# Performance work log

Measured on AMD Instinct MI355X. Metric: run time of the kernel, lower is better.

## Reference

```python
import jax, jax.numpy as jnp
import numpy as np
from jax import lax
import math

B, C_IN, C_OUT, D, H, W = 8, 32, 32, 16, 64, 64
K = 3            # kernel_size (cubic)
PAD = 1
E = 8            # num_experts
GROUPS = 1


def setup_inputs() -> dict:
    key = jax.random.key(0)
    k1, k2, k3, k4 = jax.random.split(key, 4)
    x = jax.random.normal(k1, (B, C_IN, D, H, W), dtype=jnp.float32)
    routing_weights = jax.random.uniform(k2, (B, E), dtype=jnp.float32)
    # kaiming_uniform_(a=sqrt(5)) equivalent bounds
    fan_in = (C_IN // GROUPS) * K * K * K
    gain = math.sqrt(2.0 / (1.0 + 5.0))
    w_bound = gain * math.sqrt(3.0 / fan_in)
    weight = jax.random.uniform(k3, (E, C_OUT, C_IN // GROUPS, K, K, K),
                                dtype=jnp.float32, minval=-w_bound, maxval=w_bound)
    b_bound = 1.0 / math.sqrt(fan_in)
    bias = jax.random.uniform(k4, (E, C_OUT), dtype=jnp.float32,
                              minval=-b_bound, maxval=b_bound)
    return {"x": x, "routing_weights": routing_weights, "weight": weight, "bias": bias}


def reference(x, routing_weights, weight, bias):
    # Faithful to the original einsum: 'bi,eocdwh->bocdwh' sums i and e
    # independently (outer-sum semantics), exactly as torch.einsum does.
    eff_kernel = jnp.einsum('bi,eocdwh->bocdwh', routing_weights, weight)  # [B,O,I/g,kd,kh,kw]
    eff_bias = jnp.einsum('bi,eo->bo', routing_weights, bias)              # [B,O]

    def conv_one(xi, ki, bi):
        # xi: [C_in,D,H,W]; ki: [O, I/g, kd,kh,kw]
        y = lax.conv_general_dilated(
            xi[None], ki,
            window_strides=(1, 1, 1),
            padding=[(PAD, PAD)] * 3,
            lhs_dilation=(1, 1, 1),
            rhs_dilation=(1, 1, 1),
            dimension_numbers=('NCDHW', 'OIDHW', 'NCDHW'),
            feature_group_count=GROUPS,
        )[0]
        return y + bi[:, None, None, None]

    return jax.vmap(conv_one)(x, eff_kernel, eff_bias)  # [B, C_OUT, D, H, W]
```

## Files before the change

### kernel.cpp

```cpp
#include <hip/hip_runtime.h>
#include <hip/hip_bf16.h>

typedef short short8 __attribute__((ext_vector_type(8)));
typedef float f32x4 __attribute__((ext_vector_type(4)));

#define WF_OFF  0u
#define RWB_OFF 55296u
#define RWS_OFF 56320u

#define CHS 384
#define RB  1552
#define PLANE_B (10 * RB)
#define RING_B (4 * PLANE_B)

__device__ __forceinline__ unsigned bf16rne(float f) {
    unsigned u = __float_as_uint(f);
    return (u + 0x7FFFu + ((u >> 16) & 1u)) >> 16;
}

__global__ void condconv_prep(const float* __restrict__ rw,
                              const float* __restrict__ weight,
                              const float* __restrict__ bias,
                              char* __restrict__ ws) {
    int i = blockIdx.x * 256 + threadIdx.x;
    if (i < 27648) {
        int t   = i >> 10;
        int rem = i & 1023;
        int ot  = rem >> 9;
        int l   = (rem >> 3) & 63;
        int j   = rem & 7;
        int o   = ot * 16 + (l & 15);
        int c   = 8 * (l >> 4) + j;
        float s = 0.f;
#pragma unroll
        for (int e = 0; e < 8; ++e) s += weight[((e * 32 + o) * 32 + c) * 27 + t];
        ((unsigned short*)(ws + WF_OFF))[i] = (unsigned short)bf16rne(s);
    } else if (i < 27904) {
        int k = i - 27648;
        int b = k >> 5, o = k & 31;
        float rs = 0.f, bs = 0.f;
#pragma unroll
        for (int e = 0; e < 8; ++e) { rs += rw[b * 8 + e]; bs += bias[e * 32 + o]; }
        ((float*)(ws + RWB_OFF))[k] = rs * bs;
        if (o == 0) ((float*)(ws + RWS_OFF))[b] = rs;
    }
}

__global__ __launch_bounds__(256, 2) void condconv_zwalk3(
        const float* __restrict__ x,
        const char* __restrict__ wf,
        const float* __restrict__ rwbias,
        const float* __restrict__ rwsum,
        float* __restrict__ out) {
    __shared__ __align__(16) char smem[RING_B];

    const int tid  = threadIdx.x;
    const int wv   = tid >> 6;
    const int lane = tid & 63;
    const int n    = lane & 15;
    const int quad = lane >> 4;
    const int ot   = wv & 1;
    const int yh   = wv >> 1;

    const int logical = (blockIdx.x & 7) * 64 + (blockIdx.x >> 3);
    const int b   = logical >> 6;
    const int rem = logical & 63;
    const int zb  = rem & 1;
    const int xb  = (rem >> 1) & 3;
    const int yb  = rem >> 3;
    const int y0 = yb * 8, x0 = xb * 16, zr0 = zb * 8;

    const float* xbp = x + (size_t)b * 2097152;

    const bool sact = tid < 240;
    const int  scc  = tid / 60;
    const int  rr   = tid % 60;
    const int  syp  = rr / 6;
    const int  sx4  = rr % 6;
    const int  gxq  = xb * 4 + sx4 - 1;
    const int  gy   = y0 + syp - 1;
    const bool gok  = ((unsigned)gxq < 16u) && ((unsigned)gy < 64u);
    const long soff = (long)scc * 524288 +
                      (long)(gok ? gy : 0) * 64 + (long)(gok ? gxq : 0) * 4;
    const int  woff = syp * RB + scc * CHS + (4 * sx4) * 16;

    short8 wreg[27];
    {
        const char* wb_ = wf + lane * 16 + ot * 1024;
#pragma unroll
        for (int t = 0; t < 27; ++t) wreg[t] = *(const short8*)(wb_ + t * 2048);
    }

    const float rwb = rwsum[b];
    float bb[4];
#pragma unroll
    for (int j = 0; j < 4; ++j) bb[j] = rwbias[b * 32 + ot * 16 + quad * 4 + j];
    float* outb = out + (size_t)(b * 32 + ot * 16 + quad * 4) * 65536 +
                  (size_t)(y0 + yh * 4) * 64 + x0 + n;

    auto STAGE = [&](int p) {
        if (!sact) return;
        char* pl = smem + (p & 3) * PLANE_B;
        float a[8][4];
        if (gok && (unsigned)p < 16u) {
            const float* q0 = xbp + soff + (long)p * 4096;
#pragma unroll
            for (int k = 0; k < 8; ++k) {
                const float4 v = *(const float4*)(q0 + (size_t)k * 65536);
                a[k][0] = v.x; a[k][1] = v.y; a[k][2] = v.z; a[k][3] = v.w;
            }
        } else {
#pragma unroll
            for (int k = 0; k < 8; ++k)
                { a[k][0] = 0.f; a[k][1] = 0.f; a[k][2] = 0.f; a[k][3] = 0.f; }
        }
#pragma unroll
        for (int xi = 0; xi < 4; ++xi) {
            union { __hip_bfloat162 h2[4]; uint4 u; } g;
            g.h2[0] = __float22bfloat162_rn(make_float2(a[0][xi], a[1][xi]));
            g.h2[1] = __float22bfloat162_rn(make_float2(a[2][xi], a[3][xi]));
            g.h2[2] = __float22bfloat162_rn(make_float2(a[4][xi], a[5][xi]));
            g.h2[3] = __float22bfloat162_rn(make_float2(a[6][xi], a[7][xi]));
            *(uint4*)(pl + woff + xi * 16) = g.u;
        }
    };

    STAGE(zr0 - 1);
    STAGE(zr0);

    f32x4 accA[4] = {}, accB[4] = {};

#pragma unroll 1
    for (int k = 0; k < 4; ++k) {
        const int zA = zr0 + 2 * k;

        __syncthreads();
        STAGE(zA + 1);
        STAGE(zA + 2);
        __syncthreads();

#pragma unroll
        for (int pi = 0; pi < 4; ++pi) {
            const char* Pp = smem + ((zA - 1 + pi) & 3) * PLANE_B;
#pragma unroll
            for (int q = 0; q < 6; ++q) {
                const char* rowq = Pp + (yh * 4 + q) * RB + quad * CHS;
#pragma unroll
                for (int dx = 0; dx < 3; ++dx) {
                    const int lx = n + dx + 3;
                    const short8 xf = *(const short8*)(rowq + lx * 16);
#pragma unroll
                    for (int dy = 0; dy < 3; ++dy) {
                        const int r = q - dy;
                        if (r >= 0 && r < 4) {
                            if (pi < 3)
                                accA[r] = __builtin_amdgcn_mfma_f32_16x16x32_bf16(
                                    wreg[pi * 9 + dy * 3 + dx], xf, accA[r], 0, 0, 0);
                            if (pi > 0)
                                accB[r] = __builtin_amdgcn_mfma_f32_16x16x32_bf16(
                                    wreg[(pi - 1) * 9 + dy * 3 + dx], xf, accB[r], 0, 0, 0);
                        }
                    }
                }
            }
        }

#pragma unroll
        for (int r = 0; r < 4; ++r) {
#pragma unroll
            for (int j = 0; j < 4; ++j) {
                float* po = outb + (size_t)j * 65536 + r * 64;
                po[(size_t)zA * 4096]       = rwb * accA[r][j] + bb[j];
                po[(size_t)(zA + 1) * 4096] = rwb * accB[r][j] + bb[j];
            }
            accA[r] = f32x4{0, 0, 0, 0};
            accB[r] = f32x4{0, 0, 0, 0};
        }
    }
}

extern "C" void kernel_launch(void* const* d_in, const int* in_sizes, int n_in,
                              void* d_out, int out_size, void* d_ws, size_t ws_size,
                              hipStream_t stream) {
    const float* x      = (const float*)d_in[0];
    const float* rw     = (const float*)d_in[1];
    const float* weight = (const float*)d_in[2];
    const float* bias   = (const float*)d_in[3];
    float* out = (float*)d_out;
    char*  ws  = (char*)d_ws;

    condconv_prep<<<109, 256, 0, stream>>>(rw, weight, bias, ws);
    condconv_zwalk3<<<512, 256, 0, stream>>>(
        x, ws + WF_OFF,
        (const float*)(ws + RWB_OFF), (const float*)(ws + RWS_OFF), out);
}
```

Measured before the change: 144.3 us.

## Prefetch next z-planes into registers to overlap global loads with MFMA

Splits plane staging into a global load into registers and a later LDS write, so the loads for the next two z-planes are issued before the compute phase and finish while the MFMAs run. It also replaces __syncthreads with raw s_barrier calls fenced by sched_barrier, and adds an explicit lgkmcnt wait so the barriers do not wait on outstanding global loads. The cost is 64 extra VGPRs for the prefetch buffers alongside the 27 weight registers. That pressure could cause spills under launch_bounds(256,2).

```diff
diff --git a/kernel.cpp b/kernel.cpp
--- a/kernel.cpp
+++ b/kernel.cpp
@@ -12,6 +12,11 @@
 #define RB  1552
 #define PLANE_B (10 * RB)
 #define RING_B (4 * PLANE_B)
+
+#define SCHED0() __builtin_amdgcn_sched_barrier(0)
+#define BAR_RAW()  do { SCHED0(); __builtin_amdgcn_s_barrier(); SCHED0(); } while (0)
+#define BAR_LGKM() do { SCHED0(); asm volatile("s_waitcnt lgkmcnt(0)" ::: "memory"); \
+                        __builtin_amdgcn_s_barrier(); SCHED0(); } while (0)
 
 __device__ __forceinline__ unsigned bf16rne(float f) {
     unsigned u = __float_as_uint(f);
@@ -46,7 +51,7 @@
     }
 }
 
-__global__ __launch_bounds__(256, 2) void condconv_zwalk3(
+__global__ __launch_bounds__(256, 2) void condconv_zwalk4(
         const float* __restrict__ x,
         const char* __restrict__ wf,
         const float* __restrict__ rwbias,
@@ -98,21 +103,29 @@
     float* outb = out + (size_t)(b * 32 + ot * 16 + quad * 4) * 65536 +
                   (size_t)(y0 + yh * 4) * 64 + x0 + n;
 
-    auto STAGE = [&](int p) {
+    float4 pX[8], pY[8];
+
+    auto SLOAD = [&](int p, float4 (&dst)[8]) {
+        if (!sact) return;
+        if (gok && (unsigned)p < 16u) {
+            const float* q0 = xbp + soff + (long)p * 4096;
+#pragma unroll
+            for (int kk = 0; kk < 8; ++kk)
+                dst[kk] = *(const float4*)(q0 + (size_t)kk * 65536);
+        } else {
+#pragma unroll
+            for (int kk = 0; kk < 8; ++kk)
+                dst[kk] = make_float4(0.f, 0.f, 0.f, 0.f);
+        }
+    };
+    auto SWRITE = [&](int p, const float4 (&v)[8]) {
         if (!sact) return;
         char* pl = smem + (p & 3) * PLANE_B;
         float a[8][4];
-        if (gok && (unsigned)p < 16u) {
-            const float* q0 = xbp + soff + (long)p * 4096;
-#pragma unroll
-            for (int k = 0; k < 8; ++k) {
-                const float4 v = *(const float4*)(q0 + (size_t)k * 65536);
-                a[k][0] = v.x; a[k][1] = v.y; a[k][2] = v.z; a[k][3] = v.w;
-            }
-        } else {
-#pragma unroll
-            for (int k = 0; k < 8; ++k)
-                { a[k][0] = 0.f; a[k][1] = 0.f; a[k][2] = 0.f; a[k][3] = 0.f; }
+#pragma unroll
+        for (int kk = 0; kk < 8; ++kk) {
+            a[kk][0] = v[kk].x; a[kk][1] = v[kk].y;
+            a[kk][2] = v[kk].z; a[kk][3] = v[kk].w;
         }
 #pragma unroll
         for (int xi = 0; xi < 4; ++xi) {
@@ -125,8 +138,12 @@
         }
     };
 
-    STAGE(zr0 - 1);
-    STAGE(zr0);
+    SLOAD(zr0 - 1, pX);
+    SLOAD(zr0, pY);
+    SWRITE(zr0 - 1, pX);
+    SWRITE(zr0, pY);
+    SLOAD(zr0 + 1, pX);
+    SLOAD(zr0 + 2, pY);
 
     f32x4 accA[4] = {}, accB[4] = {};
 
@@ -134,10 +151,14 @@
     for (int k = 0; k < 4; ++k) {
         const int zA = zr0 + 2 * k;
 
-        __syncthreads();
-        STAGE(zA + 1);
-        STAGE(zA + 2);
-        __syncthreads();
+        BAR_RAW();
+        SWRITE(zA + 1, pX);
+        SWRITE(zA + 2, pY);
+        if (k < 3) {
+            SLOAD(zA + 3, pX);
+            SLOAD(zA + 4, pY);
+        }
+        BAR_LGKM();
 
 #pragma unroll
         for (int pi = 0; pi < 4; ++pi) {
@@ -190,7 +211,7 @@
     char*  ws  = (char*)d_ws;
 
     condconv_prep<<<109, 256, 0, stream>>>(rw, weight, bias, ws);
-    condconv_zwalk3<<<512, 256, 0, stream>>>(
+    condconv_zwalk4<<<512, 256, 0, stream>>>(
         x, ws + WF_OFF,
         (const float*)(ws + RWB_OFF), (const float*)(ws + RWS_OFF), out);
 }
```

Measured after the change: 145.2 us. No clear change (+0.6%).
